# Optimization experiments

Hardware: AMD Instinct MI355X
Metric: run time of the kernel (lower is better)

The kernel has to match this reference:

```python
import jax, jax.numpy as jnp
import numpy as np

H = 50  # hidden size hard-coded in the torch module


def _lstm_layer(x, W_ih, W_hh, b_ih, b_hh):
    """x: [B, T, D_in] -> outputs [B, T, H]. PyTorch gate order: i, f, g, o."""
    B = x.shape[0]
    # precompute input projection for all timesteps: [B, T, 4H]
    x_proj = jnp.einsum('btd,gd->btg', x, W_ih) + b_ih + b_hh
    x_proj = jnp.swapaxes(x_proj, 0, 1)  # time-major [T, B, 4H]

    def step(carry, xt):
        h, c = carry
        gates = xt + h @ W_hh.T  # [B, 4H]
        i, f, g, o = jnp.split(gates, 4, axis=-1)
        c = jax.nn.sigmoid(f) * c + jax.nn.sigmoid(i) * jnp.tanh(g)
        h = jax.nn.sigmoid(o) * jnp.tanh(c)
        return (h, c), h

    h0 = jnp.zeros((B, H), dtype=x.dtype)
    c0 = jnp.zeros((B, H), dtype=x.dtype)
    (_, _), hs = jax.lax.scan(step, (h0, c0), x_proj)
    return jnp.swapaxes(hs, 0, 1)  # [B, T, H]


def setup_inputs() -> dict:
    key = jax.random.key(0)
    ks = jax.random.split(key, 11)
    B, T = 4096, 512
    s = 1.0 / np.sqrt(H)  # torch LSTM init scale
    return {
        'x': jax.random.normal(ks[0], (B, T, 1), dtype=jnp.float32),
        'W_ih0': jax.random.normal(ks[1], (4 * H, 1), dtype=jnp.float32) * s,
        'W_hh0': jax.random.normal(ks[2], (4 * H, H), dtype=jnp.float32) * s,
        'b_ih0': jax.random.normal(ks[3], (4 * H,), dtype=jnp.float32) * s,
        'b_hh0': jax.random.normal(ks[4], (4 * H,), dtype=jnp.float32) * s,
        'W_ih1': jax.random.normal(ks[5], (4 * H, H), dtype=jnp.float32) * s,
        'W_hh1': jax.random.normal(ks[6], (4 * H, H), dtype=jnp.float32) * s,
        'b_ih1': jax.random.normal(ks[7], (4 * H,), dtype=jnp.float32) * s,
        'b_hh1': jax.random.normal(ks[8], (4 * H,), dtype=jnp.float32) * s,
        'W_fc': jax.random.normal(ks[9], (1, H), dtype=jnp.float32) * s,
        'b_fc': jax.random.normal(ks[10], (1,), dtype=jnp.float32) * s,
    }


def reference(x, W_ih0, W_hh0, b_ih0, b_hh0, W_ih1, W_hh1, b_ih1, b_hh1, W_fc, b_fc):
    h1 = _lstm_layer(x, W_ih0, W_hh0, b_ih0, b_hh0)   # [B, T, H]
    h2 = _lstm_layer(h1, W_ih1, W_hh1, b_ih1, b_hh1)  # [B, T, H]
    last = h2[:, -1, :]                                # [B, H]
    return last @ W_fc.T + b_fc                        # [B, 1]
```

## Files before the change

### kernel.cpp

```cpp
#include <hip/hip_runtime.h>


#define TT 512
#define HH 50
#define BT 16
#define NTHR 1024
#define L2E 1.44269504f

typedef _Float16 half8 __attribute__((ext_vector_type(8)));
typedef float floatx4 __attribute__((ext_vector_type(4)));

static __device__ __forceinline__ float fexp2(float x) { return __builtin_amdgcn_exp2f(x); }
static __device__ __forceinline__ float frcp(float x)  { return __builtin_amdgcn_rcpf(x); }

static __device__ __forceinline__ float cell_update(float gi, float gf, float gg,
                                                    float go, float& c) {
    float Ei = fexp2(gi);
    float Eg = fexp2(gg);
    float Ef = fexp2(gf);
    float p1 = (1.0f + Ei) * (1.0f + Eg);
    float fe = 1.0f + Ef;
    float R  = frcp(fe * p1);
    c = R * (c * p1 + (1.0f - Eg) * fe);
    float cl = fminf(fmaxf(c, -18.0f), 18.0f);
    float Eo = fexp2(go);
    float Ec = fexp2(cl * (-2.0f * L2E));
    float Ro = frcp((1.0f + Eo) * (1.0f + Ec));
    return (1.0f - Ec) * Ro;
}

#define MFMA(a, b, c) __builtin_amdgcn_mfma_f32_16x16x32_f16((a), (b), (c), 0, 0, 0)

template<int NJ, bool WRITER>
static __device__ __forceinline__ void run_l0(
    int tbase, int ln, _Float16 (*H1)[1024], const float* xs,
    const float* __restrict__ W_ih0, const float* __restrict__ W_hh0,
    const float* __restrict__ b_ih0, const float* __restrict__ b_hh0)
{
    const int m = ln & 15, q = ln >> 4;
    const float GSC[4] = { -L2E, -L2E, -2.0f * L2E, -L2E };

    half8 a0[NJ][2];
    float c[NJ];
    int   widx[NJ];
#pragma unroll
    for (int j = 0; j < NJ; ++j) {
        const int  tau  = tbase + j;
        const int  uA   = 4 * tau + (m >> 2);
        const int  gA   = m & 3;
        const bool rokA = (uA < HH);
        const int  wrow = gA * HH + uA;
        const float sA  = GSC[gA];
#pragma unroll
        for (int ks = 0; ks < 2; ++ks) {
            half8 h8;
#pragma unroll
            for (int jj = 0; jj < 8; ++jj) {
                int k = ks * 32 + q * 8 + jj;
                float w = 0.f;
                if (rokA) {
                    if (k < HH)       w = W_hh0[wrow * HH + k];
                    else if (k == 50) w = b_ih0[wrow] + b_hh0[wrow];
                    else if (k == 51) w = W_ih0[wrow];
                }
                h8[jj] = (_Float16)(sA * w);
            }
            a0[j][ks] = h8;
        }
        const int uC = 4 * tau + q;
        const int kh = (uC < HH) ? uC : (uC + 2);
        widx[j] = ((kh >> 5) * 64 + ((kh >> 3) & 3) * 16 + m) * 8 + (kh & 7);
        c[j] = 0.f;
    }

    __syncthreads();

    {
        const float xv = xs[m];
#pragma unroll
        for (int j = 0; j < NJ; ++j) {
            const int  uC = 4 * (tbase + j) + q;
            const bool vC = (uC < HH);
            float g4[4];
#pragma unroll
            for (int g = 0; g < 4; ++g) {
                int rg = g * HH + (vC ? uC : 0);
                g4[g] = vC ? GSC[g] * ((b_ih0[rg] + b_hh0[rg]) + W_ih0[rg] * xv) : 0.f;
            }
            float h = cell_update(g4[0], g4[1], g4[2], g4[3], c[j]);
            H1[0][widx[j]] = (_Float16)h;
        }
    }
    __syncthreads();

    const floatx4 ZERO = { 0.f, 0.f, 0.f, 0.f };
    for (int s = 1; s <= 513; ++s) {
        if (s <= 511) {
            const _Float16* bufR = H1[(s - 1) & 3];
            _Float16*       bufW = H1[s & 3];
            half8 b0 = *(const half8*)&bufR[(0  + ln) * 8];
            half8 b1 = *(const half8*)&bufR[(64 + ln) * 8];
            floatx4 acc[NJ];
#pragma unroll
            for (int j = 0; j < NJ; ++j) {
                floatx4 a = MFMA(a0[j][0], b0, ZERO);
                acc[j] = MFMA(a0[j][1], b1, a);
            }
#pragma unroll
            for (int j = 0; j < NJ; ++j) {
                float h = cell_update(acc[j][0], acc[j][1], acc[j][2], acc[j][3], c[j]);
                bufW[widx[j]] = (_Float16)h;
            }
            if (WRITER) {
                if (ln < 16)
                    bufW[(96 + ln) * 8 + 3] = (_Float16)xs[(s + 1) * BT + ln];
            }
        }
        __syncthreads();
    }
}

template<int NJ>
static __device__ __forceinline__ void run_l1(
    int tbase, int ln, _Float16 (*H1)[1024], _Float16 (*H2)[1024],
    const float* __restrict__ W_ih1, const float* __restrict__ W_hh1,
    const float* __restrict__ b_ih1, const float* __restrict__ b_hh1)
{
    const int m = ln & 15, q = ln >> 4;
    const float GSC[4] = { -L2E, -L2E, -2.0f * L2E, -L2E };

    half8 a1[NJ][4];
    float c[NJ];
    int   widx[NJ];
#pragma unroll
    for (int j = 0; j < NJ; ++j) {
        const int  tau  = tbase + j;
        const int  uA   = 4 * tau + (m >> 2);
        const int  gA   = m & 3;
        const bool rokA = (uA < HH);
        const int  wrow = gA * HH + uA;
        const float sA  = GSC[gA];
#pragma unroll
        for (int ks = 0; ks < 4; ++ks) {
            half8 h8;
#pragma unroll
            for (int jj = 0; jj < 8; ++jj) {
                int k = ks * 32 + q * 8 + jj;
                float w = 0.f;
                if (rokA) {
                    if (k < HH)                      w = W_ih1[wrow * HH + k];
                    else if (k == 50)                w = b_ih1[wrow] + b_hh1[wrow];
                    else if (k >= 64 && k < 64 + HH) w = W_hh1[wrow * HH + (k - 64)];
                }
                h8[jj] = (_Float16)(sA * w);
            }
            a1[j][ks] = h8;
        }
        const int uC = 4 * tau + q;
        const int kh = (uC < HH) ? uC : (uC + 2);
        widx[j] = ((kh >> 5) * 64 + ((kh >> 3) & 3) * 16 + m) * 8 + (kh & 7);
        c[j] = 0.f;
    }

    __syncthreads();
    __syncthreads();

    half8 p0 = {}, p1 = {};
    const floatx4 ZERO = { 0.f, 0.f, 0.f, 0.f };
    for (int s = 1; s <= 513; ++s) {
        if (s >= 2) {
            const _Float16* h2R = H2[(s - 1) & 1];
            _Float16*       h2W = H2[s & 1];
            half8 b2 = *(const half8*)&h2R[(0  + ln) * 8];
            half8 b3 = *(const half8*)&h2R[(64 + ln) * 8];
            floatx4 acc[NJ];
#pragma unroll
            for (int j = 0; j < NJ; ++j) {
                floatx4 a = MFMA(a1[j][0], p0, ZERO);
                a = MFMA(a1[j][1], p1, a);
                a = MFMA(a1[j][2], b2, a);
                acc[j] = MFMA(a1[j][3], b3, a);
            }
#pragma unroll
            for (int j = 0; j < NJ; ++j) {
                float h = cell_update(acc[j][0], acc[j][1], acc[j][2], acc[j][3], c[j]);
                h2W[widx[j]] = (_Float16)h;
            }
        }
        {
            const _Float16* h1R = H1[(s - 1) & 3];
            p0 = *(const half8*)&h1R[(0  + ln) * 8];
            p1 = *(const half8*)&h1R[(64 + ln) * 8];
        }
        __syncthreads();
    }
}

__global__ __launch_bounds__(NTHR, 4) void lstm_mfma(
    const float* __restrict__ x,
    const float* __restrict__ W_ih0, const float* __restrict__ W_hh0,
    const float* __restrict__ b_ih0, const float* __restrict__ b_hh0,
    const float* __restrict__ W_ih1, const float* __restrict__ W_hh1,
    const float* __restrict__ b_ih1, const float* __restrict__ b_hh1,
    const float* __restrict__ W_fc,  const float* __restrict__ b_fc,
    float* __restrict__ out)
{
    __shared__ __align__(16) _Float16 H1[4][1024];
    __shared__ __align__(16) _Float16 H2[2][1024];
    __shared__ float xs[(TT + 1) * BT];

    const int tid = threadIdx.x;
    const int ln  = tid & 63;
    const int wv  = tid >> 6;
    const int b0g = blockIdx.x * BT;

    for (int i = tid; i < BT * TT; i += NTHR) {
        int b = i & 15, t = i >> 4;
        xs[t * BT + b] = x[(size_t)(b0g + b) * TT + t];
    }
    if (tid < BT) xs[TT * BT + tid] = 0.f;
    for (int i = tid; i < 4 * 1024; i += NTHR) ((_Float16*)H1)[i] = (_Float16)0.f;
    for (int i = tid; i < 2 * 1024; i += NTHR) ((_Float16*)H2)[i] = (_Float16)0.f;
    __syncthreads();
    if (tid < 16) {
#pragma unroll
        for (int r = 0; r < 4; ++r) H1[r][(96 + tid) * 8 + 2] = (_Float16)1.0f;
        H1[0][(96 + tid) * 8 + 3] = (_Float16)xs[BT + tid];
    }

    if (wv < 8) {
        if (wv < 5)
            run_l0<2, false>(2 * wv, ln, H1, xs, W_ih0, W_hh0, b_ih0, b_hh0);
        else if (wv < 7)
            run_l0<1, false>(10 + (wv - 5), ln, H1, xs, W_ih0, W_hh0, b_ih0, b_hh0);
        else
            run_l0<1, true>(12, ln, H1, xs, W_ih0, W_hh0, b_ih0, b_hh0);
    } else {
        const int w = wv - 8;
        if (w < 3)
            run_l1<1>(w, ln, H1, H2, W_ih1, W_hh1, b_ih1, b_hh1);
        else
            run_l1<2>(3 + 2 * (w - 3), ln, H1, H2, W_ih1, W_hh1, b_ih1, b_hh1);
    }

    if (tid < BT) {
        float a = b_fc[0];
        for (int u = 0; u < HH; ++u) {
            int idx = ((u >> 5) * 64 + ((u >> 3) & 3) * 16 + tid) * 8 + (u & 7);
            a = fmaf((float)H2[1][idx], W_fc[u], a);
        }
        out[b0g + tid] = a;
    }
}

extern "C" void kernel_launch(void* const* d_in, const int* in_sizes, int n_in,
                              void* d_out, int out_size, void* d_ws, size_t ws_size,
                              hipStream_t stream) {
    const float* x     = (const float*)d_in[0];
    const float* W_ih0 = (const float*)d_in[1];
    const float* W_hh0 = (const float*)d_in[2];
    const float* b_ih0 = (const float*)d_in[3];
    const float* b_hh0 = (const float*)d_in[4];
    const float* W_ih1 = (const float*)d_in[5];
    const float* W_hh1 = (const float*)d_in[6];
    const float* b_ih1 = (const float*)d_in[7];
    const float* b_hh1 = (const float*)d_in[8];
    const float* W_fc  = (const float*)d_in[9];
    const float* b_fc  = (const float*)d_in[10];
    float* out = (float*)d_out;

    dim3 grid(4096 / BT);
    dim3 block(NTHR);
    lstm_mfma<<<grid, block, 0, stream>>>(x, W_ih0, W_hh0, b_ih0, b_hh0,
                                          W_ih1, W_hh1, b_ih1, b_hh1,
                                          W_fc, b_fc, out);
}
```

Measured before the change: 364.5 us.

## Replace block-wide barriers with per-layer LDS progress flags and spin waits

```diff
diff --git a/kernel.cpp b/kernel.cpp
--- a/kernel.cpp
+++ b/kernel.cpp
@@ -12,6 +12,33 @@
 
 static __device__ __forceinline__ float fexp2(float x) { return __builtin_amdgcn_exp2f(x); }
 static __device__ __forceinline__ float frcp(float x)  { return __builtin_amdgcn_rcpf(x); }
+static __device__ __forceinline__ int   imin(int a, int b) { return a < b ? a : b; }
+
+static __device__ __forceinline__ int ldv(const int* p) { return *(volatile const int*)p; }
+
+static __device__ __forceinline__ void spin_ge(const int* p, int v) {
+    while (ldv(p) < v) {}
+    __asm__ volatile("" ::: "memory");
+}
+
+static __device__ __forceinline__ void publish(int* p, int v, int ln) {
+    __asm__ volatile("s_waitcnt lgkmcnt(0)" ::: "memory");
+    if (ln == 0) *(volatile int*)p = v;
+}
+
+static __device__ __forceinline__ void close_group(const int* prog, int* done,
+                                                   int v, int ln) {
+    for (;;) {
+        __asm__ volatile("" ::: "memory");
+        int4 A = *(const int4*)(prog);
+        int4 B = *(const int4*)(prog + 4);
+        int mn = imin(imin(imin(A.x, A.y), imin(A.z, A.w)),
+                      imin(imin(B.x, B.y), imin(B.z, B.w)));
+        if (mn >= v) break;
+    }
+    __asm__ volatile("" ::: "memory");
+    if (ln == 0) *(volatile int*)done = v;
+}
 
 static __device__ __forceinline__ float cell_update(float gi, float gf, float gg,
                                                     float go, float& c) {
@@ -31,9 +58,10 @@
 
 #define MFMA(a, b, c) __builtin_amdgcn_mfma_f32_16x16x32_f16((a), (b), (c), 0, 0, 0)
 
-template<int NJ, bool WRITER>
+template<int NJ, bool XW, bool CL>
 static __device__ __forceinline__ void run_l0(
-    int tbase, int ln, _Float16 (*H1)[1024], const float* xs,
+    int tbase, int gw, int ln, _Float16 (*H1)[1024], const float* xs,
+    int* prog0, int* done0, const int* done1,
     const float* __restrict__ W_ih0, const float* __restrict__ W_hh0,
     const float* __restrict__ b_ih0, const float* __restrict__ b_hh0)
 {
@@ -73,8 +101,6 @@
         c[j] = 0.f;
     }
 
-    __syncthreads();
-
     {
         const float xv = xs[m];
 #pragma unroll
@@ -90,39 +116,42 @@
             float h = cell_update(g4[0], g4[1], g4[2], g4[3], c[j]);
             H1[0][widx[j]] = (_Float16)h;
         }
-    }
-    __syncthreads();
+        publish(&prog0[gw], 1, ln);
+        if (CL) close_group(prog0, done0, 1, ln);
+    }
 
     const floatx4 ZERO = { 0.f, 0.f, 0.f, 0.f };
-    for (int s = 1; s <= 513; ++s) {
-        if (s <= 511) {
-            const _Float16* bufR = H1[(s - 1) & 3];
-            _Float16*       bufW = H1[s & 3];
-            half8 b0 = *(const half8*)&bufR[(0  + ln) * 8];
-            half8 b1 = *(const half8*)&bufR[(64 + ln) * 8];
-            floatx4 acc[NJ];
-#pragma unroll
-            for (int j = 0; j < NJ; ++j) {
-                floatx4 a = MFMA(a0[j][0], b0, ZERO);
-                acc[j] = MFMA(a0[j][1], b1, a);
-            }
-#pragma unroll
-            for (int j = 0; j < NJ; ++j) {
-                float h = cell_update(acc[j][0], acc[j][1], acc[j][2], acc[j][3], c[j]);
-                bufW[widx[j]] = (_Float16)h;
-            }
-            if (WRITER) {
-                if (ln < 16)
-                    bufW[(96 + ln) * 8 + 3] = (_Float16)xs[(s + 1) * BT + ln];
-            }
-        }
-        __syncthreads();
-    }
-}
-
-template<int NJ>
+    for (int s = 1; s <= 511; ++s) {
+        spin_ge(done0, s);
+        spin_ge(done1, s - 3);
+        const _Float16* bufR = H1[(s - 1) & 3];
+        _Float16*       bufW = H1[s & 3];
+        half8 b0 = *(const half8*)&bufR[(0  + ln) * 8];
+        half8 b1 = *(const half8*)&bufR[(64 + ln) * 8];
+        floatx4 acc[NJ];
+#pragma unroll
+        for (int j = 0; j < NJ; ++j) {
+            floatx4 a = MFMA(a0[j][0], b0, ZERO);
+            acc[j] = MFMA(a0[j][1], b1, a);
+        }
+#pragma unroll
+        for (int j = 0; j < NJ; ++j) {
+            float h = cell_update(acc[j][0], acc[j][1], acc[j][2], acc[j][3], c[j]);
+            bufW[widx[j]] = (_Float16)h;
+        }
+        if (XW) {
+            if (ln < 16)
+                bufW[(96 + ln) * 8 + 3] = (_Float16)xs[(s + 1) * BT + ln];
+        }
+        publish(&prog0[gw], s + 1, ln);
+        if (CL) close_group(prog0, done0, s + 1, ln);
+    }
+}
+
+template<int NJ, bool CL>
 static __device__ __forceinline__ void run_l1(
-    int tbase, int ln, _Float16 (*H1)[1024], _Float16 (*H2)[1024],
+    int tbase, int gw, int ln, _Float16 (*H1)[1024], _Float16 (*H2)[1024],
+    int* prog1, const int* done0, int* done1,
     const float* __restrict__ W_ih1, const float* __restrict__ W_hh1,
     const float* __restrict__ b_ih1, const float* __restrict__ b_hh1)
 {
@@ -162,37 +191,32 @@
         c[j] = 0.f;
     }
 
-    __syncthreads();
-    __syncthreads();
-
-    half8 p0 = {}, p1 = {};
     const floatx4 ZERO = { 0.f, 0.f, 0.f, 0.f };
-    for (int s = 1; s <= 513; ++s) {
-        if (s >= 2) {
-            const _Float16* h2R = H2[(s - 1) & 1];
-            _Float16*       h2W = H2[s & 1];
-            half8 b2 = *(const half8*)&h2R[(0  + ln) * 8];
-            half8 b3 = *(const half8*)&h2R[(64 + ln) * 8];
-            floatx4 acc[NJ];
-#pragma unroll
-            for (int j = 0; j < NJ; ++j) {
-                floatx4 a = MFMA(a1[j][0], p0, ZERO);
-                a = MFMA(a1[j][1], p1, a);
-                a = MFMA(a1[j][2], b2, a);
-                acc[j] = MFMA(a1[j][3], b3, a);
-            }
-#pragma unroll
-            for (int j = 0; j < NJ; ++j) {
-                float h = cell_update(acc[j][0], acc[j][1], acc[j][2], acc[j][3], c[j]);
-                h2W[widx[j]] = (_Float16)h;
-            }
-        }
-        {
-            const _Float16* h1R = H1[(s - 1) & 3];
-            p0 = *(const half8*)&h1R[(0  + ln) * 8];
-            p1 = *(const half8*)&h1R[(64 + ln) * 8];
-        }
-        __syncthreads();
+    for (int u = 0; u <= 511; ++u) {
+        spin_ge(done0, u + 1);
+        spin_ge(done1, u);
+        const _Float16* h1R = H1[u & 3];
+        const _Float16* h2R = H2[(u + 1) & 1];
+        _Float16*       h2W = H2[u & 1];
+        half8 p0 = *(const half8*)&h1R[(0  + ln) * 8];
+        half8 p1 = *(const half8*)&h1R[(64 + ln) * 8];
+        half8 b2 = *(const half8*)&h2R[(0  + ln) * 8];
+        half8 b3 = *(const half8*)&h2R[(64 + ln) * 8];
+        floatx4 acc[NJ];
+#pragma unroll
+        for (int j = 0; j < NJ; ++j) {
+            floatx4 a = MFMA(a1[j][0], p0, ZERO);
+            a = MFMA(a1[j][1], p1, a);
+            a = MFMA(a1[j][2], b2, a);
+            acc[j] = MFMA(a1[j][3], b3, a);
+        }
+#pragma unroll
+        for (int j = 0; j < NJ; ++j) {
+            float h = cell_update(acc[j][0], acc[j][1], acc[j][2], acc[j][3], c[j]);
+            h2W[widx[j]] = (_Float16)h;
+        }
+        publish(&prog1[gw], u + 1, ln);
+        if (CL) close_group(prog1, done1, u + 1, ln);
     }
 }
 
@@ -208,6 +232,8 @@
     __shared__ __align__(16) _Float16 H1[4][1024];
     __shared__ __align__(16) _Float16 H2[2][1024];
     __shared__ float xs[(TT + 1) * BT];
+    __shared__ __align__(16) int prog0[8], prog1[8];
+    __shared__ int gdone[2];
 
     const int tid = threadIdx.x;
     const int ln  = tid & 63;
@@ -221,29 +247,49 @@
     if (tid < BT) xs[TT * BT + tid] = 0.f;
     for (int i = tid; i < 4 * 1024; i += NTHR) ((_Float16*)H1)[i] = (_Float16)0.f;
     for (int i = tid; i < 2 * 1024; i += NTHR) ((_Float16*)H2)[i] = (_Float16)0.f;
+    if (tid < 8)  { prog0[tid] = 0; prog1[tid] = 0; }
+    if (tid < 2)  gdone[tid] = 0;
     __syncthreads();
     if (tid < 16) {
 #pragma unroll
         for (int r = 0; r < 4; ++r) H1[r][(96 + tid) * 8 + 2] = (_Float16)1.0f;
         H1[0][(96 + tid) * 8 + 3] = (_Float16)xs[BT + tid];
     }
+    __syncthreads();
 
     if (wv < 8) {
         if (wv < 5)
-            run_l0<2, false>(2 * wv, ln, H1, xs, W_ih0, W_hh0, b_ih0, b_hh0);
-        else if (wv < 7)
-            run_l0<1, false>(10 + (wv - 5), ln, H1, xs, W_ih0, W_hh0, b_ih0, b_hh0);
+            run_l0<2, false, false>(2 * wv, wv, ln, H1, xs,
+                                    prog0, &gdone[0], &gdone[1],
+                                    W_ih0, W_hh0, b_ih0, b_hh0);
+        else if (wv == 5)
+            run_l0<1, false, true>(10, 5, ln, H1, xs,
+                                   prog0, &gdone[0], &gdone[1],
+                                   W_ih0, W_hh0, b_ih0, b_hh0);
+        else if (wv == 6)
+            run_l0<1, true, false>(11, 6, ln, H1, xs,
+                                   prog0, &gdone[0], &gdone[1],
+                                   W_ih0, W_hh0, b_ih0, b_hh0);
         else
-            run_l0<1, true>(12, ln, H1, xs, W_ih0, W_hh0, b_ih0, b_hh0);
+            run_l0<1, false, false>(12, 7, ln, H1, xs,
+                                    prog0, &gdone[0], &gdone[1],
+                                    W_ih0, W_hh0, b_ih0, b_hh0);
     } else {
         const int w = wv - 8;
-        if (w < 3)
-            run_l1<1>(w, ln, H1, H2, W_ih1, W_hh1, b_ih1, b_hh1);
+        if (w == 1)
+            run_l1<1, true>(1, 1, ln, H1, H2, prog1, &gdone[0], &gdone[1],
+                            W_ih1, W_hh1, b_ih1, b_hh1);
+        else if (w < 3)
+            run_l1<1, false>(w, w, ln, H1, H2, prog1, &gdone[0], &gdone[1],
+                             W_ih1, W_hh1, b_ih1, b_hh1);
         else
-            run_l1<2>(3 + 2 * (w - 3), ln, H1, H2, W_ih1, W_hh1, b_ih1, b_hh1);
+            run_l1<2, false>(3 + 2 * (w - 3), w, ln, H1, H2,
+                             prog1, &gdone[0], &gdone[1],
+                             W_ih1, W_hh1, b_ih1, b_hh1);
     }
 
     if (tid < BT) {
+        spin_ge(&gdone[1], 512);
         float a = b_fc[0];
         for (int u = 0; u < HH; ++u) {
             int idx = ((u >> 5) * 64 + ((u >> 3) & 3) * 16 + tid) * 8 + (u & 7);
```

Measured after the change: 454.3 us. 1.25x slower.

## Replace block-wide barriers with LDS counter-based producer/consumer sync between LSTM layers

Applied to the files above, without the earlier changes.

```diff
diff --git a/kernel.cpp b/kernel.cpp
--- a/kernel.cpp
+++ b/kernel.cpp
@@ -12,6 +12,22 @@
 
 static __device__ __forceinline__ float fexp2(float x) { return __builtin_amdgcn_exp2f(x); }
 static __device__ __forceinline__ float frcp(float x)  { return __builtin_amdgcn_rcpf(x); }
+
+static __device__ __forceinline__ void wait2(const int* cnt, int need0, int need1) {
+    int a = ((volatile const int*)cnt)[0];
+    int b = ((volatile const int*)cnt)[1];
+    while (a < need0 || b < need1) {
+        __builtin_amdgcn_s_sleep(1);
+        a = ((volatile const int*)cnt)[0];
+        b = ((volatile const int*)cnt)[1];
+    }
+    __asm__ volatile("" ::: "memory");
+}
+
+static __device__ __forceinline__ void publish(int* p, int ln) {
+    __asm__ volatile("s_waitcnt lgkmcnt(0)" ::: "memory");
+    if (ln == 0) atomicAdd(p, 1);
+}
 
 static __device__ __forceinline__ float cell_update(float gi, float gf, float gg,
                                                     float go, float& c) {
@@ -31,9 +47,9 @@
 
 #define MFMA(a, b, c) __builtin_amdgcn_mfma_f32_16x16x32_f16((a), (b), (c), 0, 0, 0)
 
-template<int NJ, bool WRITER>
+template<int NJ, bool XW>
 static __device__ __forceinline__ void run_l0(
-    int tbase, int ln, _Float16 (*H1)[1024], const float* xs,
+    int tbase, int ln, _Float16 (*H1)[1024], const float* xs, int* cnt,
     const float* __restrict__ W_ih0, const float* __restrict__ W_hh0,
     const float* __restrict__ b_ih0, const float* __restrict__ b_hh0)
 {
@@ -73,8 +89,6 @@
         c[j] = 0.f;
     }
 
-    __syncthreads();
-
     {
         const float xv = xs[m];
 #pragma unroll
@@ -90,39 +104,53 @@
             float h = cell_update(g4[0], g4[1], g4[2], g4[3], c[j]);
             H1[0][widx[j]] = (_Float16)h;
         }
-    }
-    __syncthreads();
+        publish(&cnt[0], ln);
+    }
 
     const floatx4 ZERO = { 0.f, 0.f, 0.f, 0.f };
-    for (int s = 1; s <= 513; ++s) {
-        if (s <= 511) {
-            const _Float16* bufR = H1[(s - 1) & 3];
-            _Float16*       bufW = H1[s & 3];
-            half8 b0 = *(const half8*)&bufR[(0  + ln) * 8];
-            half8 b1 = *(const half8*)&bufR[(64 + ln) * 8];
-            floatx4 acc[NJ];
-#pragma unroll
-            for (int j = 0; j < NJ; ++j) {
-                floatx4 a = MFMA(a0[j][0], b0, ZERO);
-                acc[j] = MFMA(a0[j][1], b1, a);
-            }
-#pragma unroll
-            for (int j = 0; j < NJ; ++j) {
-                float h = cell_update(acc[j][0], acc[j][1], acc[j][2], acc[j][3], c[j]);
-                bufW[widx[j]] = (_Float16)h;
-            }
-            if (WRITER) {
-                if (ln < 16)
-                    bufW[(96 + ln) * 8 + 3] = (_Float16)xs[(s + 1) * BT + ln];
-            }
-        }
-        __syncthreads();
-    }
+
+#define L0STEP(SS, RB, WB)                                                  \
+    {                                                                       \
+        const int s_ = (SS);                                                \
+        wait2(cnt, 8 * s_, 8 * (s_ - 3));                                   \
+        const _Float16* bufR = H1[(RB)];                                    \
+        _Float16*       bufW = H1[(WB)];                                    \
+        half8 b0 = *(const half8*)&bufR[(0  + ln) * 8];                     \
+        half8 b1 = *(const half8*)&bufR[(64 + ln) * 8];                     \
+        floatx4 acc[NJ];                                                    \
+        _Pragma("unroll")                                                   \
+        for (int j = 0; j < NJ; ++j) {                                      \
+            floatx4 a = MFMA(a0[j][0], b0, ZERO);                           \
+            acc[j] = MFMA(a0[j][1], b1, a);                                 \
+        }                                                                   \
+        _Pragma("unroll")                                                   \
+        for (int j = 0; j < NJ; ++j) {                                      \
+            float h = cell_update(acc[j][0], acc[j][1], acc[j][2], acc[j][3], c[j]); \
+            bufW[widx[j]] = (_Float16)h;                                    \
+        }                                                                   \
+        if (XW) {                                                           \
+            if (ln < 16)             \
+                bufW[(96 + ln) * 8 + 3] = (_Float16)xs[(s_ + 1) * BT + ln]; \
+        }                                                                   \
+        publish(&cnt[0], ln);                                               \
+    }
+
+    for (int k = 0; k < 127; ++k) {
+        const int s0 = 4 * k + 1;
+        L0STEP(s0,     0, 1);
+        L0STEP(s0 + 1, 1, 2);
+        L0STEP(s0 + 2, 2, 3);
+        L0STEP(s0 + 3, 3, 0);
+    }
+    L0STEP(509, 0, 1);
+    L0STEP(510, 1, 2);
+    L0STEP(511, 2, 3);
+#undef L0STEP
 }
 
 template<int NJ>
 static __device__ __forceinline__ void run_l1(
-    int tbase, int ln, _Float16 (*H1)[1024], _Float16 (*H2)[1024],
+    int tbase, int ln, _Float16 (*H1)[1024], _Float16 (*H2)[1024], int* cnt,
     const float* __restrict__ W_ih1, const float* __restrict__ W_hh1,
     const float* __restrict__ b_ih1, const float* __restrict__ b_hh1)
 {
@@ -162,38 +190,43 @@
         c[j] = 0.f;
     }
 
-    __syncthreads();
-    __syncthreads();
-
-    half8 p0 = {}, p1 = {};
     const floatx4 ZERO = { 0.f, 0.f, 0.f, 0.f };
-    for (int s = 1; s <= 513; ++s) {
-        if (s >= 2) {
-            const _Float16* h2R = H2[(s - 1) & 1];
-            _Float16*       h2W = H2[s & 1];
-            half8 b2 = *(const half8*)&h2R[(0  + ln) * 8];
-            half8 b3 = *(const half8*)&h2R[(64 + ln) * 8];
-            floatx4 acc[NJ];
-#pragma unroll
-            for (int j = 0; j < NJ; ++j) {
-                floatx4 a = MFMA(a1[j][0], p0, ZERO);
-                a = MFMA(a1[j][1], p1, a);
-                a = MFMA(a1[j][2], b2, a);
-                acc[j] = MFMA(a1[j][3], b3, a);
-            }
-#pragma unroll
-            for (int j = 0; j < NJ; ++j) {
-                float h = cell_update(acc[j][0], acc[j][1], acc[j][2], acc[j][3], c[j]);
-                h2W[widx[j]] = (_Float16)h;
-            }
-        }
-        {
-            const _Float16* h1R = H1[(s - 1) & 3];
-            p0 = *(const half8*)&h1R[(0  + ln) * 8];
-            p1 = *(const half8*)&h1R[(64 + ln) * 8];
-        }
-        __syncthreads();
-    }
+
+#define L1STEP(UU, RB1, RB2, WB2)                                           \
+    {                                                                       \
+        const int u_ = (UU);                                                \
+        wait2(cnt, 8 * (u_ + 1), 8 * u_);                                   \
+        const _Float16* h1R = H1[(RB1)];                                    \
+        const _Float16* h2R = H2[(RB2)];                                    \
+        _Float16*       h2W = H2[(WB2)];                                    \
+        half8 p0 = *(const half8*)&h1R[(0  + ln) * 8];                      \
+        half8 p1 = *(const half8*)&h1R[(64 + ln) * 8];                      \
+        half8 b2 = *(const half8*)&h2R[(0  + ln) * 8];                      \
+        half8 b3 = *(const half8*)&h2R[(64 + ln) * 8];                      \
+        floatx4 acc[NJ];                                                    \
+        _Pragma("unroll")                                                   \
+        for (int j = 0; j < NJ; ++j) {                                      \
+            floatx4 a = MFMA(a1[j][0], p0, ZERO);                           \
+            a = MFMA(a1[j][1], p1, a);                                      \
+            a = MFMA(a1[j][2], b2, a);                                      \
+            acc[j] = MFMA(a1[j][3], b3, a);                                 \
+        }                                                                   \
+        _Pragma("unroll")                                                   \
+        for (int j = 0; j < NJ; ++j) {                                      \
+            float h = cell_update(acc[j][0], acc[j][1], acc[j][2], acc[j][3], c[j]); \
+            h2W[widx[j]] = (_Float16)h;                                     \
+        }                                                                   \
+        publish(&cnt[1], ln);                                               \
+    }
+
+    for (int k = 0; k < 128; ++k) {
+        const int u0 = 4 * k;
+        L1STEP(u0,     0, 1, 0);
+        L1STEP(u0 + 1, 1, 0, 1);
+        L1STEP(u0 + 2, 2, 1, 0);
+        L1STEP(u0 + 3, 3, 0, 1);
+    }
+#undef L1STEP
 }
 
 __global__ __launch_bounds__(NTHR, 4) void lstm_mfma(
@@ -208,6 +241,7 @@
     __shared__ __align__(16) _Float16 H1[4][1024];
     __shared__ __align__(16) _Float16 H2[2][1024];
     __shared__ float xs[(TT + 1) * BT];
+    __shared__ __align__(8) int cnt[2];
 
     const int tid = threadIdx.x;
     const int ln  = tid & 63;
@@ -221,29 +255,34 @@
     if (tid < BT) xs[TT * BT + tid] = 0.f;
     for (int i = tid; i < 4 * 1024; i += NTHR) ((_Float16*)H1)[i] = (_Float16)0.f;
     for (int i = tid; i < 2 * 1024; i += NTHR) ((_Float16*)H2)[i] = (_Float16)0.f;
+    if (tid < 2) cnt[tid] = 0;
     __syncthreads();
     if (tid < 16) {
 #pragma unroll
         for (int r = 0; r < 4; ++r) H1[r][(96 + tid) * 8 + 2] = (_Float16)1.0f;
         H1[0][(96 + tid) * 8 + 3] = (_Float16)xs[BT + tid];
     }
+    __syncthreads();
 
     if (wv < 8) {
         if (wv < 5)
-            run_l0<2, false>(2 * wv, ln, H1, xs, W_ih0, W_hh0, b_ih0, b_hh0);
-        else if (wv < 7)
-            run_l0<1, false>(10 + (wv - 5), ln, H1, xs, W_ih0, W_hh0, b_ih0, b_hh0);
+            run_l0<2, false>(2 * wv, ln, H1, xs, cnt, W_ih0, W_hh0, b_ih0, b_hh0);
+        else if (wv == 6)
+            run_l0<1, true>(11, ln, H1, xs, cnt, W_ih0, W_hh0, b_ih0, b_hh0);
         else
-            run_l0<1, true>(12, ln, H1, xs, W_ih0, W_hh0, b_ih0, b_hh0);
+            run_l0<1, false>(wv == 5 ? 10 : 12, ln, H1, xs, cnt,
+                             W_ih0, W_hh0, b_ih0, b_hh0);
     } else {
         const int w = wv - 8;
         if (w < 3)
-            run_l1<1>(w, ln, H1, H2, W_ih1, W_hh1, b_ih1, b_hh1);
+            run_l1<1>(w, ln, H1, H2, cnt, W_ih1, W_hh1, b_ih1, b_hh1);
         else
-            run_l1<2>(3 + 2 * (w - 3), ln, H1, H2, W_ih1, W_hh1, b_ih1, b_hh1);
+            run_l1<2>(3 + 2 * (w - 3), ln, H1, H2, cnt,
+                      W_ih1, W_hh1, b_ih1, b_hh1);
     }
 
     if (tid < BT) {
+        wait2(cnt, 0, 8 * 512);
         float a = b_fc[0];
         for (int u = 0; u < HH; ++u) {
             int idx = ((u >> 5) * 64 + ((u >> 3) & 3) * 16 + tid) * 8 + (u & 7);
```

After: 412.3 us. +13.1%, slower.
